# Performance work log

Measured on AMD Instinct MI355X. Metric: run time of the kernel, lower is better.

## Reference

```python
import jax, jax.numpy as jnp
import numpy as np

H = 16
DK = 64
D_MODEL = H * DK  # 1024
WORD_DIM = 768


def setup_inputs() -> dict:
    key = jax.random.key(0)
    ks = jax.random.split(key, 12)
    B, S = 8, 1024
    s = 0.02
    return {
        "query": jax.random.normal(ks[0], (B, S, WORD_DIM), jnp.float32),
        "key": jax.random.normal(ks[1], (B, S, WORD_DIM), jnp.float32),
        "value": jax.random.normal(ks[2], (B, S, WORD_DIM), jnp.float32),
        "Wq": jax.random.normal(ks[3], (WORD_DIM, D_MODEL), jnp.float32) * s,
        "bq": jnp.zeros((D_MODEL,), jnp.float32),
        "Wk": jax.random.normal(ks[4], (WORD_DIM, D_MODEL), jnp.float32) * s,
        "bk": jnp.zeros((D_MODEL,), jnp.float32),
        "Wv": jax.random.normal(ks[5], (WORD_DIM, D_MODEL), jnp.float32) * s,
        "bv": jnp.zeros((D_MODEL,), jnp.float32),
        "Wo": jax.random.normal(ks[6], (D_MODEL, D_MODEL), jnp.float32) * s,
        "bo": jnp.zeros((D_MODEL,), jnp.float32),
    }


def _split_heads(x):
    # [B, S, d_model] -> [B, H, S, DK]
    B, S, _ = x.shape
    return x.reshape(B, S, H, DK).transpose(0, 2, 1, 3)


def reference(query, key, value, Wq, bq, Wk, bk, Wv, bv, Wo, bo):
    q = _split_heads(query @ Wq + bq)
    k = _split_heads(key @ Wk + bk)
    v = _split_heads(value @ Wv + bv)
    scores = jnp.einsum("bhqd,bhkd->bhqk", q, k) / jnp.sqrt(jnp.float32(DK))
    p_attn = jax.nn.softmax(scores, axis=-1)  # [B, H, S, S]
    x = jnp.einsum("bhqk,bhkd->bhqd", p_attn, v)
    B, _, S, _ = x.shape
    x = x.transpose(0, 2, 1, 3).reshape(B, S, D_MODEL)
    out = x @ Wo + bo
    return out, p_attn
```

## Files before the change

### kernel.cpp

```cpp
#include <hip/hip_runtime.h>
#include <hip/hip_bf16.h>
#include <cstdint>
#include <cstddef>


#define H_ 16
#define DK_ 64
#define DM_ 1024
#define WD_ 768
#define B_ 8
#define S_ 1024

typedef float f32x4 __attribute__((ext_vector_type(4)));
typedef __bf16 bf16x8 __attribute__((ext_vector_type(8)));
typedef short s16x8 __attribute__((ext_vector_type(8)));

__device__ __forceinline__ unsigned short f2bf(float x) {
  unsigned int u = __builtin_bit_cast(unsigned int, x);
  u += 0x7FFFu + ((u >> 16) & 1u);
  return (unsigned short)(u >> 16);
}

__device__ __forceinline__ float bf2f(unsigned short b) {
  return __builtin_bit_cast(float, (unsigned int)b << 16);
}

__device__ __forceinline__ f32x4 mfma16(bf16x8 a, bf16x8 b, f32x4 c) {
  return __builtin_amdgcn_mfma_f32_16x16x32_bf16(a, b, c, 0, 0, 0);
}

__device__ __forceinline__ bf16x8 ld_bf8(const unsigned short* p) {
  return *reinterpret_cast<const bf16x8*>(p);
}

__device__ __forceinline__ void nt_store_f4(float* p, f32x4 v) {
  __builtin_nontemporal_store(v, reinterpret_cast<f32x4*>(p));
}

__device__ __forceinline__ int xcd_swz(int wg, int n) {
  int q = n >> 3;
  return (wg & 7) * q + (wg >> 3);
}

#define GLOAD_LDS16(g, l)                                            \
  __builtin_amdgcn_global_load_lds(                                  \
      (const __attribute__((address_space(1))) void*)(g),            \
      (__attribute__((address_space(3))) void*)(l), 16, 0, 0)

__device__ __forceinline__ bf16x8 lds_frag(const unsigned short* base, int row, int cb) {
  return *reinterpret_cast<const bf16x8*>(
      reinterpret_cast<const char*>(base) + row * 128 + (cb ^ ((row & 7) << 4)));
}

__global__ void k_conv3(const float* __restrict__ q, const float* __restrict__ k,
                        const float* __restrict__ v, unsigned short* __restrict__ qo,
                        unsigned short* __restrict__ ko, unsigned short* __restrict__ vo,
                        int n) {
  const float* in = blockIdx.y == 0 ? q : blockIdx.y == 1 ? k : v;
  unsigned short* out = blockIdx.y == 0 ? qo : blockIdx.y == 1 ? ko : vo;
  int i0 = (blockIdx.x * blockDim.x + threadIdx.x) * 8;
  int stride = gridDim.x * blockDim.x * 8;
  for (int i = i0; i < n; i += stride) {
    float4 a = *reinterpret_cast<const float4*>(in + i);
    float4 b = *reinterpret_cast<const float4*>(in + i + 4);
    s16x8 o;
    o[0] = (short)f2bf(a.x); o[1] = (short)f2bf(a.y);
    o[2] = (short)f2bf(a.z); o[3] = (short)f2bf(a.w);
    o[4] = (short)f2bf(b.x); o[5] = (short)f2bf(b.y);
    o[6] = (short)f2bf(b.z); o[7] = (short)f2bf(b.w);
    *reinterpret_cast<s16x8*>(out + i) = o;
  }
}

__global__ void k_tconvA(const float* __restrict__ Wq, const float* __restrict__ Wk,
                         const float* __restrict__ Wv, const float* __restrict__ Wo,
                         unsigned short* __restrict__ Wqt, unsigned short* __restrict__ Wkt,
                         unsigned short* __restrict__ Wvt, unsigned short* __restrict__ Wot) {
  __shared__ float tt[32][33];
  const int z = blockIdx.z;
  const float* W = z == 0 ? Wq : z == 1 ? Wk : z == 2 ? Wv : Wo;
  unsigned short* Wt = z == 0 ? Wqt : z == 1 ? Wkt : z == 2 ? Wvt : Wot;
  const int KW = (z == 3) ? DM_ : WD_;
  const int k0 = blockIdx.y * 32;
  if (k0 >= KW) return;
  const int n0 = blockIdx.x * 32;
  int tx = threadIdx.x, ty = threadIdx.y;
  for (int dy = ty; dy < 32; dy += 8)
    tt[dy][tx] = W[(size_t)(k0 + dy) * DM_ + n0 + tx];
  __syncthreads();
  for (int dy = ty; dy < 32; dy += 8)
    Wt[(size_t)(n0 + dy) * KW + k0 + tx] = f2bf(tt[tx][dy]);
}

template <int MODE, int KD>
__global__ __launch_bounds__(256, 3) void k_mm(
    const unsigned short* __restrict__ A0, const unsigned short* __restrict__ A1,
    const unsigned short* __restrict__ A2, const unsigned short* __restrict__ B0,
    const unsigned short* __restrict__ B1, const unsigned short* __restrict__ B2,
    const float* __restrict__ bias0, const float* __restrict__ bias1,
    const float* __restrict__ bias2, unsigned short* __restrict__ O0,
    unsigned short* __restrict__ O1, unsigned short* __restrict__ O2,
    float* __restrict__ Of) {
  const int z = blockIdx.z;
  const unsigned short* A = z == 0 ? A0 : z == 1 ? A1 : A2;
  const unsigned short* Bt = z == 0 ? B0 : z == 1 ? B1 : B2;
  const float* bias = z == 0 ? bias0 : z == 1 ? bias1 : bias2;

  const int nbn = (MODE == 0 && z == 2) ? 64 : 8;
  const int swz = xcd_swz(blockIdx.x, 512);
  const int m0 = (swz / nbn) * 128, n0 = (swz % nbn) * 128;

  __shared__ unsigned short As[8192];
  __shared__ unsigned short Bs[8192];

  const int t = threadIdx.x;
  const int lane = t & 63, w = t >> 6;
  const int l16 = lane & 15, lhi = lane >> 4;
  const int wm = (w >> 1) * 64, wn = (w & 1) * 64;

  f32x4 acc[4][4] = {};

  const int rs0 = t >> 3;
  const int cb0 = (t & 7) << 4;

  for (int k0 = 0; k0 < KD; k0 += 64) {
#pragma unroll
    for (int i = 0; i < 4; ++i) {
      const int r = rs0 + i * 32;
      const int cb = cb0 ^ ((r & 7) << 4);
      const unsigned short* Ag;
      if (MODE == 2) {
        Ag = A + ((size_t)((m0 >> 10) * 16 + (k0 >> 6)) * 1024 + (m0 & 1023) + r) * 64 +
             (cb >> 1);
      } else {
        Ag = A + (size_t)(m0 + r) * KD + k0 + (cb >> 1);
      }
      GLOAD_LDS16(Ag, As + w * 512 + i * 2048);
      GLOAD_LDS16(Bt + (size_t)(n0 + r) * KD + k0 + (cb >> 1),
                  Bs + w * 512 + i * 2048);
    }
    __syncthreads();
#pragma unroll
    for (int ksub = 0; ksub < 2; ++ksub) {
      bf16x8 aF[4], bF[4];
#pragma unroll
      for (int i = 0; i < 4; ++i)
        aF[i] = lds_frag(As, wm + i * 16 + l16, ksub * 64 + lhi * 16);
#pragma unroll
      for (int j = 0; j < 4; ++j)
        bF[j] = lds_frag(Bs, wn + j * 16 + l16, ksub * 64 + lhi * 16);
#pragma unroll
      for (int i = 0; i < 4; ++i)
#pragma unroll
        for (int j = 0; j < 4; ++j)
          acc[i][j] = mfma16(bF[j], aF[i], acc[i][j]);
    }
    __syncthreads();
  }

#pragma unroll
  for (int i = 0; i < 4; ++i) {
#pragma unroll
    for (int j = 0; j < 4; ++j) {
      if (MODE == 2) {
        int m = m0 + wm + i * 16 + l16;
        int nb = n0 + wn + j * 16 + lhi * 4;
        float4 bb = *reinterpret_cast<const float4*>(&bias[nb]);
        f32x4 o;
        o[0] = acc[i][j][0] + bb.x;
        o[1] = acc[i][j][1] + bb.y;
        o[2] = acc[i][j][2] + bb.z;
        o[3] = acc[i][j][3] + bb.w;
        nt_store_f4(&Of[(size_t)m * DM_ + nb], o);
      } else if (z < 2) {
        int m = m0 + wm + i * 16 + l16;
        int nb = n0 + wn + j * 16 + lhi * 4;
        float4 bb = *reinterpret_cast<const float4*>(&bias[nb]);
        ushort4 o;
        o.x = f2bf(acc[i][j][0] + bb.x);
        o.y = f2bf(acc[i][j][1] + bb.y);
        o.z = f2bf(acc[i][j][2] + bb.z);
        o.w = f2bf(acc[i][j][3] + bb.w);
        unsigned short* Ob = z ? O1 : O0;
        *reinterpret_cast<ushort4*>(&Ob[(size_t)m * DM_ + nb]) = o;
      } else {
        int R = m0 + wm + i * 16 + l16;
        int Ms = n0 + wn + j * 16 + lhi * 4;
        int b = Ms >> 10, s = Ms & (S_ - 1);
        float bn = bias[R];
        ushort4 o;
        o.x = f2bf(acc[i][j][0] + bn);
        o.y = f2bf(acc[i][j][1] + bn);
        o.z = f2bf(acc[i][j][2] + bn);
        o.w = f2bf(acc[i][j][3] + bn);
        *reinterpret_cast<ushort4*>(
            &O2[((size_t)(b * 1024 + R)) * (size_t)S_ + s]) = o;
      }
    }
  }
}

__global__ __launch_bounds__(512, 4) void k_attn(
    const unsigned short* __restrict__ Qb, const unsigned short* __restrict__ Kb,
    const unsigned short* __restrict__ Vt, float* __restrict__ P,
    unsigned short* __restrict__ Xh) {
  __shared__ unsigned short Plds[32][1032];
  __shared__ float red[32][8];
  __shared__ float rowS[32];
  const int t = threadIdx.x;
  const int lane = t & 63, wid = t >> 6;
  const int l16 = lane & 15, lhi = lane >> 4;

  const int swz = xcd_swz(blockIdx.y * gridDim.x + blockIdx.x,
                          gridDim.x * gridDim.y);
  const int bh = swz >> 5;
  const int q0 = (swz & 31) * 32;
  const int b = bh >> 4, h = bh & 15;
  const unsigned short* Qbase = Qb + ((size_t)(b * S_ + q0) * DM_ + h * DK_);
  const unsigned short* Kbase = Kb + ((size_t)(b * S_) * DM_ + h * DK_);

  f32x4 acc[2][8] = {};
  const int n0 = wid * 128;
#pragma unroll
  for (int ks = 0; ks < 2; ++ks) {
    bf16x8 qf[2];
#pragma unroll
    for (int i = 0; i < 2; ++i)
      qf[i] = ld_bf8(Qbase + (size_t)(i * 16 + l16) * DM_ + ks * 32 + lhi * 8);
#pragma unroll
    for (int j = 0; j < 8; ++j) {
      bf16x8 kf = ld_bf8(Kbase + (size_t)(n0 + j * 16 + l16) * DM_ + ks * 32 + lhi * 8);
#pragma unroll
      for (int i = 0; i < 2; ++i)
        acc[i][j] = mfma16(kf, qf[i], acc[i][j]);
    }
  }

#pragma unroll
  for (int i = 0; i < 2; ++i) {
    float s = 0.f;
#pragma unroll
    for (int j = 0; j < 8; ++j)
#pragma unroll
      for (int r = 0; r < 4; ++r) {
        float e = __expf(acc[i][j][r] * 0.125f);
        acc[i][j][r] = e;
        s += e;
      }
    s += __shfl_xor(s, 16);
    s += __shfl_xor(s, 32);
    if (lane < 16) red[i * 16 + l16][wid] = s;
  }
  __syncthreads();
  if (t < 32) {
    float s = red[t][0];
#pragma unroll
    for (int w = 1; w < 8; ++w) s += red[t][w];
    rowS[t] = s;
  }
  __syncthreads();

#pragma unroll
  for (int i = 0; i < 2; ++i) {
    float inv = 1.f / rowS[i * 16 + l16];
#pragma unroll
    for (int j = 0; j < 8; ++j) {
      f32x4 v = acc[i][j] * inv;
      ushort4 pb;
      pb.x = f2bf(v[0]); pb.y = f2bf(v[1]);
      pb.z = f2bf(v[2]); pb.w = f2bf(v[3]);
      *reinterpret_cast<ushort4*>(&Plds[i * 16 + l16][n0 + j * 16 + lhi * 4]) = pb;
    }
  }
  __syncthreads();

  const int i2 = wid >> 2, j2 = wid & 3;
  const unsigned short* Vrow = Vt + ((size_t)bh * DK_ + j2 * 16 + l16) * S_;
  f32x4 acc0 = {}, acc1 = {};
#pragma unroll 4
  for (int k0 = 0; k0 < S_; k0 += 64) {
    bf16x8 a0 = ld_bf8(&Plds[i2 * 16 + l16][k0 + lhi * 8]);
    bf16x8 v0 = ld_bf8(Vrow + k0 + lhi * 8);
    acc0 = mfma16(a0, v0, acc0);
    bf16x8 a1 = ld_bf8(&Plds[i2 * 16 + l16][k0 + 32 + lhi * 8]);
    bf16x8 v1 = ld_bf8(Vrow + k0 + 32 + lhi * 8);
    acc1 = mfma16(a1, v1, acc1);
  }
  acc0 += acc1;

  {
    float* Prow0 = P + ((size_t)bh * S_ + q0) * S_;
#pragma unroll
    for (int rr = 0; rr < 4; ++rr) {
      int q = wid * 4 + rr;
#pragma unroll
      for (int c = 0; c < 4; ++c) {
        ushort4 pv = *reinterpret_cast<const ushort4*>(&Plds[q][c * 256 + lane * 4]);
        f32x4 o;
        o[0] = bf2f(pv.x); o[1] = bf2f(pv.y);
        o[2] = bf2f(pv.z); o[3] = bf2f(pv.w);
        nt_store_f4(&Prow0[(size_t)q * S_ + c * 256 + lane * 4], o);
      }
    }
  }
  __syncthreads();

  unsigned short* Xs = &Plds[0][0];
#pragma unroll
  for (int r = 0; r < 4; ++r) {
    int row = i2 * 16 + lhi * 4 + r;
    Xs[row * 72 + j2 * 16 + l16] = f2bf(acc0[r]);
  }
  __syncthreads();
  if (t < 256) {
    int row = t >> 3, l8 = t & 7;
    s16x8 xv = *reinterpret_cast<const s16x8*>(&Xs[row * 72 + l8 * 8]);
    *reinterpret_cast<s16x8*>(
        &Xh[((size_t)(b * H_ + h) * S_ + q0 + row) * DK_ + l8 * 8]) = xv;
  }
}


extern "C" void kernel_launch(void* const* d_in, const int* in_sizes, int n_in,
                              void* d_out, int out_size, void* d_ws, size_t ws_size,
                              hipStream_t stream) {
  const float* query = (const float*)d_in[0];
  const float* key   = (const float*)d_in[1];
  const float* value = (const float*)d_in[2];
  const float* Wq = (const float*)d_in[3];
  const float* bq = (const float*)d_in[4];
  const float* Wk = (const float*)d_in[5];
  const float* bk = (const float*)d_in[6];
  const float* Wv = (const float*)d_in[7];
  const float* bv = (const float*)d_in[8];
  const float* Wo = (const float*)d_in[9];
  const float* bo = (const float*)d_in[10];

  char* ws = (char*)d_ws;
  size_t off = 0;
  auto alloc = [&](size_t bytes) {
    void* p = ws + off;
    off += (bytes + 255) & ~(size_t)255;
    return p;
  };
  unsigned short* qb  = (unsigned short*)alloc((size_t)B_ * S_ * WD_ * 2);
  unsigned short* kb  = (unsigned short*)alloc((size_t)B_ * S_ * WD_ * 2);
  unsigned short* vb  = (unsigned short*)alloc((size_t)B_ * S_ * WD_ * 2);
  unsigned short* Wqt = (unsigned short*)alloc((size_t)DM_ * WD_ * 2);
  unsigned short* Wkt = (unsigned short*)alloc((size_t)DM_ * WD_ * 2);
  unsigned short* Wvt = (unsigned short*)alloc((size_t)DM_ * WD_ * 2);
  unsigned short* Wot = (unsigned short*)alloc((size_t)DM_ * DM_ * 2);
  unsigned short* Qb  = (unsigned short*)alloc((size_t)B_ * S_ * DM_ * 2);
  unsigned short* Kb  = (unsigned short*)alloc((size_t)B_ * S_ * DM_ * 2);
  unsigned short* Vt  = (unsigned short*)alloc((size_t)B_ * H_ * DK_ * S_ * 2);
  unsigned short* Xh  = (unsigned short*)alloc((size_t)B_ * H_ * S_ * DK_ * 2);

  float* out = (float*)d_out;
  float* P = out + (size_t)B_ * S_ * DM_;

  const int nAct = B_ * S_ * WD_;
  k_conv3<<<dim3(1024, 3), 256, 0, stream>>>(query, key, value, qb, kb, vb, nAct);
  k_tconvA<<<dim3(32, 32, 4), dim3(32, 8), 0, stream>>>(
      Wq, Wk, Wv, Wo, Wqt, Wkt, Wvt, Wot);

  k_mm<0, WD_><<<dim3(512, 1, 3), 256, 0, stream>>>(
      qb, kb, Wvt, Wqt, Wkt, vb, bq, bk, bv, Qb, Kb, Vt, nullptr);

  k_attn<<<dim3(32, 128), 512, 0, stream>>>(Qb, Kb, Vt, P, Xh);

  k_mm<2, DM_><<<dim3(512, 1, 1), 256, 0, stream>>>(
      Xh, nullptr, nullptr, Wot, nullptr, nullptr, bo, nullptr, nullptr,
      nullptr, nullptr, nullptr, out);
}
```

Before: 332.1 us.

## Specialize warps: half compute PV, half stream P to global

The attention kernel's tail is split by warp role. Four warps now compute the P·V product, each covering two row tiles and reusing its V loads, and write X directly to global memory. The other four warps store the fp32 P matrix concurrently. This removes two block barriers and the LDS staging of X, and overlaps the large P store with the PV MFMAs. The trade-off is that X is written with scattered 2-byte stores, and the MFMA work is packed into fewer warps.

New measurement: 275.7 us (median of 2 runs). -17.0%, faster.

```diff
diff --git a/kernel.cpp b/kernel.cpp
--- a/kernel.cpp
+++ b/kernel.cpp
@@ -274,25 +274,37 @@
   }
   __syncthreads();
 
-  const int i2 = wid >> 2, j2 = wid & 3;
-  const unsigned short* Vrow = Vt + ((size_t)bh * DK_ + j2 * 16 + l16) * S_;
-  f32x4 acc0 = {}, acc1 = {};
+  if (wid < 4) {
+    const int j2 = wid;
+    const unsigned short* Vrow = Vt + ((size_t)bh * DK_ + j2 * 16 + l16) * S_;
+    f32x4 pacc[2][2] = {};
 #pragma unroll 4
-  for (int k0 = 0; k0 < S_; k0 += 64) {
-    bf16x8 a0 = ld_bf8(&Plds[i2 * 16 + l16][k0 + lhi * 8]);
-    bf16x8 v0 = ld_bf8(Vrow + k0 + lhi * 8);
-    acc0 = mfma16(a0, v0, acc0);
-    bf16x8 a1 = ld_bf8(&Plds[i2 * 16 + l16][k0 + 32 + lhi * 8]);
-    bf16x8 v1 = ld_bf8(Vrow + k0 + 32 + lhi * 8);
-    acc1 = mfma16(a1, v1, acc1);
-  }
-  acc0 += acc1;
-
-  {
+    for (int k0 = 0; k0 < S_; k0 += 64) {
+      bf16x8 v0 = ld_bf8(Vrow + k0 + lhi * 8);
+      bf16x8 v1 = ld_bf8(Vrow + k0 + 32 + lhi * 8);
+#pragma unroll
+      for (int i2 = 0; i2 < 2; ++i2) {
+        bf16x8 a0 = ld_bf8(&Plds[i2 * 16 + l16][k0 + lhi * 8]);
+        bf16x8 a1 = ld_bf8(&Plds[i2 * 16 + l16][k0 + 32 + lhi * 8]);
+        pacc[i2][0] = mfma16(a0, v0, pacc[i2][0]);
+        pacc[i2][1] = mfma16(a1, v1, pacc[i2][1]);
+      }
+    }
+#pragma unroll
+    for (int i2 = 0; i2 < 2; ++i2) {
+      f32x4 x = pacc[i2][0] + pacc[i2][1];
+#pragma unroll
+      for (int r = 0; r < 4; ++r) {
+        int s = q0 + i2 * 16 + lhi * 4 + r;
+        Xh[((size_t)(b * H_ + h) * S_ + s) * DK_ + j2 * 16 + l16] = f2bf(x[r]);
+      }
+    }
+  } else {
     float* Prow0 = P + ((size_t)bh * S_ + q0) * S_;
-#pragma unroll
-    for (int rr = 0; rr < 4; ++rr) {
-      int q = wid * 4 + rr;
+    const int qbase = (wid - 4) * 8;
+#pragma unroll
+    for (int rr = 0; rr < 8; ++rr) {
+      int q = qbase + rr;
 #pragma unroll
       for (int c = 0; c < 4; ++c) {
         ushort4 pv = *reinterpret_cast<const ushort4*>(&Plds[q][c * 256 + lane * 4]);
@@ -302,21 +314,6 @@
         nt_store_f4(&Prow0[(size_t)q * S_ + c * 256 + lane * 4], o);
       }
     }
-  }
-  __syncthreads();
-
-  unsigned short* Xs = &Plds[0][0];
-#pragma unroll
-  for (int r = 0; r < 4; ++r) {
-    int row = i2 * 16 + lhi * 4 + r;
-    Xs[row * 72 + j2 * 16 + l16] = f2bf(acc0[r]);
-  }
-  __syncthreads();
-  if (t < 256) {
-    int row = t >> 3, l8 = t & 7;
-    s16x8 xv = *reinterpret_cast<const s16x8*>(&Xs[row * 72 + l8 * 8]);
-    *reinterpret_cast<s16x8*>(
-        &Xh[((size_t)(b * H_ + h) * S_ + q0 + row) * DK_ + l8 * 8]) = xv;
   }
 }
 
```
